# Optimization experiments

Hardware: AMD Instinct MI355X
Metric: run time of the kernel (lower is better)

The kernel has to match this reference:

```python
import jax, jax.numpy as jnp
import numpy as np

B = 512
D_MODEL = 512
D_STATE = 128
D_CONV = 2
EXPAND = 2
D_INNER = EXPAND * D_MODEL          # 1024
DT_RANK = (D_MODEL + 15) // 16      # 32 (mamba default 'auto')
HIDDEN = 256


def setup_inputs() -> dict:
    key = jax.random.key(0)
    ks = jax.random.split(key, 12)
    s = 0.02
    f32 = jnp.float32
    inp = {
        "x": jax.random.normal(ks[0], (B, D_MODEL), f32),
        # Mamba params (torch Linear weight layout: [out, in])
        "in_proj_w": jax.random.normal(ks[1], (2 * D_INNER, D_MODEL), f32) * s,
        "conv_w": jax.random.normal(ks[2], (D_INNER, D_CONV), f32) * s,  # depthwise kernel
        "conv_b": jnp.zeros((D_INNER,), f32),
        "x_proj_w": jax.random.normal(ks[3], (DT_RANK + 2 * D_STATE, D_INNER), f32) * s,
        "dt_proj_w": jax.random.normal(ks[4], (D_INNER, DT_RANK), f32) * s,
        "dt_proj_b": jax.random.normal(ks[5], (D_INNER,), f32) * s,
        "A_log": jnp.log(jnp.broadcast_to(
            jnp.arange(1, D_STATE + 1, dtype=f32), (D_INNER, D_STATE)).copy()),
        "D": jnp.ones((D_INNER,), f32),
        "out_proj_w": jax.random.normal(ks[6], (D_MODEL, D_INNER), f32) * s,
        # head params
        "fc1_w": jax.random.normal(ks[7], (HIDDEN, D_MODEL), f32) * s,
        "fc1_b": jnp.zeros((HIDDEN,), f32),
        "fc5_w": jax.random.normal(ks[8], (1, HIDDEN), f32) * s,
        "fc5_b": jnp.zeros((1,), f32),
    }
    return inp


def _mamba(x3, in_proj_w, conv_w, conv_b, x_proj_w, dt_proj_w, dt_proj_b,
           A_log, D, out_proj_w):
    # x3: [B, L, d_model]
    Bn, L, _ = x3.shape
    xz = jnp.einsum('bld,ed->ble', x3, in_proj_w)          # [B, L, 2*d_inner]
    xin, z = xz[..., :D_INNER], xz[..., D_INNER:]
    # depthwise causal conv1d (kernel D_CONV, padding D_CONV-1, truncated to L)
    xp = jnp.pad(xin, ((0, 0), (D_CONV - 1, 0), (0, 0)))
    conv = conv_b
    for k in range(D_CONV):
        conv = conv + conv_w[:, k] * xp[:, k:k + L, :]
    xin = jax.nn.silu(conv)                                 # [B, L, d_inner]
    x_dbl = jnp.einsum('blc,ec->ble', xin, x_proj_w)        # [B, L, dt_rank+2*d_state]
    dt = x_dbl[..., :DT_RANK]
    Bm = x_dbl[..., DT_RANK:DT_RANK + D_STATE]              # [B, L, d_state]
    Cm = x_dbl[..., DT_RANK + D_STATE:]                     # [B, L, d_state]
    dt = jax.nn.softplus(jnp.einsum('blr,cr->blc', dt, dt_proj_w) + dt_proj_b)
    A = -jnp.exp(A_log)                                     # [d_inner, d_state]
    dA = jnp.exp(dt[..., None] * A)                         # [B, L, d_inner, d_state]
    dBu = dt[..., None] * Bm[:, :, None, :] * xin[..., None]

    def step(h, t):
        dA_t, dBu_t, C_t = t
        h = dA_t * h + dBu_t                                # [B, d_inner, d_state]
        y_t = jnp.einsum('bcs,bs->bc', h, C_t)
        return h, y_t

    h0 = jnp.zeros((Bn, D_INNER, D_STATE), x3.dtype)
    _, ys = jax.lax.scan(step, h0, (dA.transpose(1, 0, 2, 3),
                                    dBu.transpose(1, 0, 2, 3),
                                    Cm.transpose(1, 0, 2)))
    y = ys.transpose(1, 0, 2)                               # [B, L, d_inner]
    y = (y + D * xin) * jax.nn.silu(z)
    return jnp.einsum('blc,dc->bld', y, out_proj_w)         # [B, L, d_model]


def reference(x, in_proj_w, conv_w, conv_b, x_proj_w, dt_proj_w, dt_proj_b,
              A_log, D, out_proj_w, fc1_w, fc1_b, fc5_w, fc5_b):
    h = _mamba(x[:, None, :], in_proj_w, conv_w, conv_b, x_proj_w,
               dt_proj_w, dt_proj_b, A_log, D, out_proj_w)[:, 0, :]
    h = h @ fc1_w.T + fc1_b
    h = jnp.where(h >= 0, h, 0.1 * h)   # LeakyReLU(0.1); dropout is eval-mode identity
    h = h @ fc5_w.T + fc5_b
    return jax.nn.sigmoid(h)            # [B, 1]
```

## Files before the change

kernel.cpp:

```cpp
#include <hip/hip_runtime.h>
#include <hip/hip_bf16.h>
#include <cstddef>

typedef __attribute__((ext_vector_type(8))) short short8;
typedef __attribute__((ext_vector_type(4))) float f32x4;

#define MFMA16(a, b, c) __builtin_amdgcn_mfma_f32_16x16x32_bf16((a), (b), (c), 0, 0, 0)

static __device__ __forceinline__ unsigned short f2bf(float f) {
    unsigned int u = __float_as_uint(f);
    u = (u + 0x7FFFu + ((u >> 16) & 1u)) >> 16;
    return (unsigned short)u;
}
static __device__ __forceinline__ float bf2f(unsigned short h) {
    return __uint_as_float(((unsigned int)h) << 16);
}
static __device__ __forceinline__ float silu_f(float v) { return v / (1.f + expf(-v)); }

enum : size_t {
    O_X    = 0,
    O_WIP  = O_X    + 512 * 512,
    O_WXP  = O_WIP  + 2048 * 512,
    O_WDT  = O_WXP  + 288 * 1024,
    O_WOUT = O_WDT  + 1024 * 32,
    O_WFC1 = O_WOUT + 512 * 1024,
    O_XIN  = O_WFC1 + 256 * 512,
    O_SZ   = O_XIN  + 512 * 1024,
    O_XDBL = O_SZ   + 512 * 1024,
    O_Y    = O_XDBL + 512 * 288,
    O_MOUT = O_Y    + 512 * 1024,
};

static __device__ __forceinline__ void cvt_seg(const float* __restrict__ s,
                                               unsigned short* __restrict__ d,
                                               int n, int gt, int np)
{
    for (int i = gt * 4; i < n; i += np * 4) {
        float4 v = *reinterpret_cast<const float4*>(s + i);
        ushort4 o;
        o.x = f2bf(v.x); o.y = f2bf(v.y); o.z = f2bf(v.z); o.w = f2bf(v.w);
        *reinterpret_cast<ushort4*>(d + i) = o;
    }
}

__global__ __launch_bounds__(256) void k_convert(
    const float* __restrict__ x,    const float* __restrict__ wip,
    const float* __restrict__ wxp,  const float* __restrict__ wdt,
    const float* __restrict__ wout, const float* __restrict__ wfc1,
    unsigned short* __restrict__ dst)
{
    const int gt = blockIdx.x * blockDim.x + threadIdx.x;
    const int np = gridDim.x * blockDim.x;
    cvt_seg(x,    dst + O_X,    512 * 512,  gt, np);
    cvt_seg(wip,  dst + O_WIP,  2048 * 512, gt, np);
    cvt_seg(wxp,  dst + O_WXP,  288 * 1024, gt, np);
    cvt_seg(wdt,  dst + O_WDT,  1024 * 32,  gt, np);
    cvt_seg(wout, dst + O_WOUT, 512 * 1024, gt, np);
    cvt_seg(wfc1, dst + O_WFC1, 256 * 512,  gt, np);
}

__global__ __launch_bounds__(256, 2) void k_s1(
    unsigned short* __restrict__ wsb,
    const float* __restrict__ cw, const float* __restrict__ cb)
{
    const int tid = threadIdx.x;
    const int w = tid >> 6, lane = tid & 63, l15 = lane & 15, g = lane >> 4;
    const int n0 = blockIdx.x * 64;
    const int m0 = blockIdx.y * 64 + w * 16;

    const unsigned short* ab = wsb + O_X   + (size_t)(m0 + l15) * 512 + g * 8;
    const unsigned short* bb = wsb + O_WIP + (size_t)(n0 + l15) * 512 + g * 8;

    f32x4 acc[4] = {};
#pragma unroll 4
    for (int k0 = 0; k0 < 512; k0 += 32) {
        short8 a = *reinterpret_cast<const short8*>(ab + k0);
#pragma unroll
        for (int f = 0; f < 4; ++f) {
            short8 b = *reinterpret_cast<const short8*>(bb + f * 16 * 512 + k0);
            acc[f] = MFMA16(a, b, acc[f]);
        }
    }

    const bool xhalf = (n0 < 1024);
    unsigned short* dst = wsb + (xhalf ? O_XIN : O_SZ);
#pragma unroll
    for (int f = 0; f < 4; ++f) {
        int n = n0 + f * 16 + l15;
        int c = xhalf ? n : n - 1024;
        float cwv = 0.f, cbv = 0.f;
        if (xhalf) { cwv = cw[2 * n + 1]; cbv = cb[n]; }
#pragma unroll
        for (int i = 0; i < 4; ++i) {
            int r = m0 + g * 4 + i;
            float v = acc[f][i];
            v = xhalf ? silu_f(cbv + cwv * v) : silu_f(v);
            dst[(size_t)r * 1024 + c] = f2bf(v);
        }
    }
}

__global__ __launch_bounds__(256, 2) void k_s2(unsigned short* __restrict__ wsb)
{
    const int tid = threadIdx.x;
    const int w = tid >> 6, lane = tid & 63, l15 = lane & 15, g = lane >> 4;
    const int n0 = blockIdx.x * 16;
    const int m0 = blockIdx.y * 64 + w * 16;

    const unsigned short* ab = wsb + O_XIN + (size_t)(m0 + l15) * 1024 + g * 8;
    const unsigned short* bb = wsb + O_WXP + (size_t)(n0 + l15) * 1024 + g * 8;

    f32x4 acc = {};
#pragma unroll 4
    for (int k0 = 0; k0 < 1024; k0 += 32) {
        short8 a = *reinterpret_cast<const short8*>(ab + k0);
        short8 b = *reinterpret_cast<const short8*>(bb + k0);
        acc = MFMA16(a, b, acc);
    }
    unsigned short* xd = wsb + O_XDBL;
#pragma unroll
    for (int i = 0; i < 4; ++i)
        xd[(size_t)(m0 + g * 4 + i) * 288 + n0 + l15] = f2bf(acc[i]);
}

__global__ __launch_bounds__(256, 2) void k_s3(
    unsigned short* __restrict__ wsb,
    const float* __restrict__ dtb, const float* __restrict__ Dv)
{
    __shared__ float bcp[16][17];
    __shared__ float bc_s[16];
    const int tid = threadIdx.x;
    const int w = tid >> 6, lane = tid & 63, l15 = lane & 15, g = lane >> 4;
    const int n0 = blockIdx.x * 256;
    const int m0 = blockIdx.y * 16;

    const unsigned short* xd = wsb + O_XDBL;
    {
        int r = tid >> 4, p = tid & 15;
        const unsigned short* row = xd + (size_t)(m0 + r) * 288;
        float s = 0.f;
#pragma unroll
        for (int q = 0; q < 8; ++q)
            s += bf2f(row[32 + p * 8 + q]) * bf2f(row[160 + p * 8 + q]);
        bcp[r][p] = s;
    }
    short8 a = *reinterpret_cast<const short8*>(xd + (size_t)(m0 + l15) * 288 + g * 8);
    __syncthreads();
    if (tid < 16) {
        float s = 0.f;
#pragma unroll
        for (int p = 0; p < 16; ++p) s += bcp[tid][p];
        bc_s[tid] = s;
    }
    __syncthreads();

    const unsigned short* wdtb = wsb + O_WDT;
    const unsigned short* xinb = wsb + O_XIN;
    const unsigned short* szb  = wsb + O_SZ;
    unsigned short* yb = wsb + O_Y;
    const f32x4 z4 = {0.f, 0.f, 0.f, 0.f};
#pragma unroll
    for (int f = 0; f < 4; ++f) {
        int n = n0 + w * 64 + f * 16 + l15;
        short8 b = *reinterpret_cast<const short8*>(wdtb + (size_t)n * 32 + g * 8);
        f32x4 acc = MFMA16(a, b, z4);
        float dtbv = dtb[n], Dvv = Dv[n];
#pragma unroll
        for (int i = 0; i < 4; ++i) {
            int r = m0 + g * 4 + i;
            float dtv = acc[i] + dtbv;
            dtv = (dtv > 20.f) ? dtv : log1pf(expf(dtv));
            float yv = bf2f(xinb[(size_t)r * 1024 + n]) *
                       (dtv * bc_s[g * 4 + i] + Dvv) *
                       bf2f(szb[(size_t)r * 1024 + n]);
            yb[(size_t)r * 1024 + n] = f2bf(yv);
        }
    }
}

__global__ __launch_bounds__(256, 2) void k_s4(unsigned short* __restrict__ wsb)
{
    const int tid = threadIdx.x;
    const int w = tid >> 6, lane = tid & 63, l15 = lane & 15, g = lane >> 4;
    const int n0 = blockIdx.x * 64 + w * 16;
    const int m0 = blockIdx.y * 16;

    const unsigned short* ab = wsb + O_Y    + (size_t)(m0 + l15) * 1024 + g * 8;
    const unsigned short* bb = wsb + O_WOUT + (size_t)(n0 + l15) * 1024 + g * 8;

    f32x4 acc = {};
#pragma unroll 4
    for (int k0 = 0; k0 < 1024; k0 += 32) {
        short8 a = *reinterpret_cast<const short8*>(ab + k0);
        short8 b = *reinterpret_cast<const short8*>(bb + k0);
        acc = MFMA16(a, b, acc);
    }
    unsigned short* mo = wsb + O_MOUT;
#pragma unroll
    for (int i = 0; i < 4; ++i)
        mo[(size_t)(m0 + g * 4 + i) * 512 + n0 + l15] = f2bf(acc[i]);
}

__global__ __launch_bounds__(256, 2) void k_s5(
    unsigned short* __restrict__ wsb,
    const float* __restrict__ bfc1, const float* __restrict__ wfc5,
    const float* __restrict__ bfc5, float* __restrict__ out)
{
    __shared__ float red[16][72];
    const int tid = threadIdx.x;
    const int w = tid >> 6, lane = tid & 63, l15 = lane & 15, g = lane >> 4;
    const int m0 = blockIdx.x * 16;

    const unsigned short* ab = wsb + O_MOUT + (size_t)(m0 + l15) * 512 + g * 8;
    const unsigned short* bb = wsb + O_WFC1 + (size_t)(w * 64 + l15) * 512 + g * 8;

    f32x4 acc[4] = {};
#pragma unroll 4
    for (int k0 = 0; k0 < 512; k0 += 32) {
        short8 a = *reinterpret_cast<const short8*>(ab + k0);
#pragma unroll
        for (int f = 0; f < 4; ++f) {
            short8 b = *reinterpret_cast<const short8*>(bb + f * 16 * 512 + k0);
            acc[f] = MFMA16(a, b, acc[f]);
        }
    }
    float part[4] = {0.f, 0.f, 0.f, 0.f};
#pragma unroll
    for (int f = 0; f < 4; ++f) {
        int n = w * 64 + f * 16 + l15;
        float b1 = bfc1[n], w5 = wfc5[n];
#pragma unroll
        for (int i = 0; i < 4; ++i) {
            float v = acc[f][i] + b1;
            v = v >= 0.f ? v : 0.1f * v;
            part[i] = fmaf(v, w5, part[i]);
        }
    }
#pragma unroll
    for (int i = 0; i < 4; ++i) red[g * 4 + i][w * 16 + l15] = part[i];
    __syncthreads();
    if (tid < 16) {
        float s = 0.f;
        for (int j = 0; j < 64; ++j) s += red[tid][j];
        out[m0 + tid] = 1.f / (1.f + expf(-(s + bfc5[0])));
    }
}

extern "C" void kernel_launch(void* const* d_in, const int* in_sizes, int n_in,
                              void* d_out, int out_size, void* d_ws, size_t ws_size,
                              hipStream_t stream)
{
    const float* x    = (const float*)d_in[0];
    const float* wip  = (const float*)d_in[1];
    const float* cw   = (const float*)d_in[2];
    const float* cb   = (const float*)d_in[3];
    const float* wxp  = (const float*)d_in[4];
    const float* wdt  = (const float*)d_in[5];
    const float* bdt  = (const float*)d_in[6];
    const float* Dv   = (const float*)d_in[8];
    const float* wout = (const float*)d_in[9];
    const float* wfc1 = (const float*)d_in[10];
    const float* bfc1 = (const float*)d_in[11];
    const float* wfc5 = (const float*)d_in[12];
    const float* bfc5 = (const float*)d_in[13];
    float* out = (float*)d_out;

    unsigned short* wsb = (unsigned short*)d_ws;

    k_convert<<<dim3(512),   256, 0, stream>>>(x, wip, wxp, wdt, wout, wfc1, wsb);
    k_s1     <<<dim3(32, 8), 256, 0, stream>>>(wsb, cw, cb);
    k_s2     <<<dim3(18, 8), 256, 0, stream>>>(wsb);
    k_s3     <<<dim3(4, 32), 256, 0, stream>>>(wsb, bdt, Dv);
    k_s4     <<<dim3(8, 32), 256, 0, stream>>>(wsb);
    k_s5     <<<dim3(32),    256, 0, stream>>>(wsb, bfc1, wfc5, bfc5, out);
}
```

Measured before the change: 147.7 us.

## Fuse fp32-to-bf16 conversion into GEMM loads and merge s3/s4 kernels

Removes the separate conversion kernel. Each GEMM now reads fp32 weights and inputs directly and packs them to bf16 in registers with v_cvt_pk_bf16_f32. The y computation (s3) is fused into the out_proj GEMM (s4) through an LDS tile, so y no longer round-trips through global memory and one launch is dropped. The head kernel moves to 512 threads with a shuffle reduction. The cost is that the fused kernel recomputes the dt/y tile in each of the 8 column blocks, and fp32 weights (twice the bytes) are re-read by many blocks instead of once.

```diff
diff --git a/kernel.cpp b/kernel.cpp
--- a/kernel.cpp
+++ b/kernel.cpp
@@ -17,67 +17,44 @@
 }
 static __device__ __forceinline__ float silu_f(float v) { return v / (1.f + expf(-v)); }
 
+static __device__ __forceinline__ short8 cvt_frag(const float* __restrict__ p) {
+    float4 a = *reinterpret_cast<const float4*>(p);
+    float4 b = *reinterpret_cast<const float4*>(p + 4);
+    union { short8 s; unsigned int u[4]; } r;
+    asm("v_cvt_pk_bf16_f32 %0, %1, %2" : "=v"(r.u[0]) : "v"(a.x), "v"(a.y));
+    asm("v_cvt_pk_bf16_f32 %0, %1, %2" : "=v"(r.u[1]) : "v"(a.z), "v"(a.w));
+    asm("v_cvt_pk_bf16_f32 %0, %1, %2" : "=v"(r.u[2]) : "v"(b.x), "v"(b.y));
+    asm("v_cvt_pk_bf16_f32 %0, %1, %2" : "=v"(r.u[3]) : "v"(b.z), "v"(b.w));
+    return r.s;
+}
+
 enum : size_t {
-    O_X    = 0,
-    O_WIP  = O_X    + 512 * 512,
-    O_WXP  = O_WIP  + 2048 * 512,
-    O_WDT  = O_WXP  + 288 * 1024,
-    O_WOUT = O_WDT  + 1024 * 32,
-    O_WFC1 = O_WOUT + 512 * 1024,
-    O_XIN  = O_WFC1 + 256 * 512,
+    O_XIN  = 0,
     O_SZ   = O_XIN  + 512 * 1024,
     O_XDBL = O_SZ   + 512 * 1024,
-    O_Y    = O_XDBL + 512 * 288,
-    O_MOUT = O_Y    + 512 * 1024,
+    O_MOUT = O_XDBL + 512 * 288,
 };
 
-static __device__ __forceinline__ void cvt_seg(const float* __restrict__ s,
-                                               unsigned short* __restrict__ d,
-                                               int n, int gt, int np)
-{
-    for (int i = gt * 4; i < n; i += np * 4) {
-        float4 v = *reinterpret_cast<const float4*>(s + i);
-        ushort4 o;
-        o.x = f2bf(v.x); o.y = f2bf(v.y); o.z = f2bf(v.z); o.w = f2bf(v.w);
-        *reinterpret_cast<ushort4*>(d + i) = o;
-    }
-}
-
-__global__ __launch_bounds__(256) void k_convert(
-    const float* __restrict__ x,    const float* __restrict__ wip,
-    const float* __restrict__ wxp,  const float* __restrict__ wdt,
-    const float* __restrict__ wout, const float* __restrict__ wfc1,
-    unsigned short* __restrict__ dst)
-{
-    const int gt = blockIdx.x * blockDim.x + threadIdx.x;
-    const int np = gridDim.x * blockDim.x;
-    cvt_seg(x,    dst + O_X,    512 * 512,  gt, np);
-    cvt_seg(wip,  dst + O_WIP,  2048 * 512, gt, np);
-    cvt_seg(wxp,  dst + O_WXP,  288 * 1024, gt, np);
-    cvt_seg(wdt,  dst + O_WDT,  1024 * 32,  gt, np);
-    cvt_seg(wout, dst + O_WOUT, 512 * 1024, gt, np);
-    cvt_seg(wfc1, dst + O_WFC1, 256 * 512,  gt, np);
-}
-
 __global__ __launch_bounds__(256, 2) void k_s1(
-    unsigned short* __restrict__ wsb,
-    const float* __restrict__ cw, const float* __restrict__ cb)
+    const float* __restrict__ x, const float* __restrict__ wip,
+    const float* __restrict__ cw, const float* __restrict__ cb,
+    unsigned short* __restrict__ wsb)
 {
     const int tid = threadIdx.x;
     const int w = tid >> 6, lane = tid & 63, l15 = lane & 15, g = lane >> 4;
     const int n0 = blockIdx.x * 64;
     const int m0 = blockIdx.y * 64 + w * 16;
 
-    const unsigned short* ab = wsb + O_X   + (size_t)(m0 + l15) * 512 + g * 8;
-    const unsigned short* bb = wsb + O_WIP + (size_t)(n0 + l15) * 512 + g * 8;
+    const float* arow = x   + (size_t)(m0 + l15) * 512 + g * 8;
+    const float* brow = wip + (size_t)(n0 + l15) * 512 + g * 8;
 
     f32x4 acc[4] = {};
 #pragma unroll 4
     for (int k0 = 0; k0 < 512; k0 += 32) {
-        short8 a = *reinterpret_cast<const short8*>(ab + k0);
+        short8 a = cvt_frag(arow + k0);
 #pragma unroll
         for (int f = 0; f < 4; ++f) {
-            short8 b = *reinterpret_cast<const short8*>(bb + f * 16 * 512 + k0);
+            short8 b = cvt_frag(brow + (size_t)f * 16 * 512 + k0);
             acc[f] = MFMA16(a, b, acc[f]);
         }
     }
@@ -100,7 +77,8 @@
     }
 }
 
-__global__ __launch_bounds__(256, 2) void k_s2(unsigned short* __restrict__ wsb)
+__global__ __launch_bounds__(256, 2) void k_s2(
+    const float* __restrict__ wxp, unsigned short* __restrict__ wsb)
 {
     const int tid = threadIdx.x;
     const int w = tid >> 6, lane = tid & 63, l15 = lane & 15, g = lane >> 4;
@@ -108,13 +86,13 @@
     const int m0 = blockIdx.y * 64 + w * 16;
 
     const unsigned short* ab = wsb + O_XIN + (size_t)(m0 + l15) * 1024 + g * 8;
-    const unsigned short* bb = wsb + O_WXP + (size_t)(n0 + l15) * 1024 + g * 8;
+    const float* brow = wxp + (size_t)(n0 + l15) * 1024 + g * 8;
 
     f32x4 acc = {};
 #pragma unroll 4
     for (int k0 = 0; k0 < 1024; k0 += 32) {
         short8 a = *reinterpret_cast<const short8*>(ab + k0);
-        short8 b = *reinterpret_cast<const short8*>(bb + k0);
+        short8 b = cvt_frag(brow + k0);
         acc = MFMA16(a, b, acc);
     }
     unsigned short* xd = wsb + O_XDBL;
@@ -123,15 +101,17 @@
         xd[(size_t)(m0 + g * 4 + i) * 288 + n0 + l15] = f2bf(acc[i]);
 }
 
-__global__ __launch_bounds__(256, 2) void k_s3(
-    unsigned short* __restrict__ wsb,
-    const float* __restrict__ dtb, const float* __restrict__ Dv)
-{
+__global__ __launch_bounds__(256, 2) void k_s34(
+    const float* __restrict__ wdt, const float* __restrict__ dtb,
+    const float* __restrict__ Dv,  const float* __restrict__ wout,
+    unsigned short* __restrict__ wsb)
+{
+    __shared__ __align__(16) unsigned short y_lds[16 * 1032];
     __shared__ float bcp[16][17];
     __shared__ float bc_s[16];
-    const int tid = threadIdx.x;
-    const int w = tid >> 6, lane = tid & 63, l15 = lane & 15, g = lane >> 4;
-    const int n0 = blockIdx.x * 256;
+
+    const int tid = threadIdx.x;
+    const int w = tid >> 6, lane = tid & 63, l15 = lane & 15, g = lane >> 4;
     const int m0 = blockIdx.y * 16;
 
     const unsigned short* xd = wsb + O_XDBL;
@@ -144,7 +124,7 @@
             s += bf2f(row[32 + p * 8 + q]) * bf2f(row[160 + p * 8 + q]);
         bcp[r][p] = s;
     }
-    short8 a = *reinterpret_cast<const short8*>(xd + (size_t)(m0 + l15) * 288 + g * 8);
+    short8 a3 = *reinterpret_cast<const short8*>(xd + (size_t)(m0 + l15) * 288 + g * 8);
     __syncthreads();
     if (tid < 16) {
         float s = 0.f;
@@ -154,45 +134,35 @@
     }
     __syncthreads();
 
-    const unsigned short* wdtb = wsb + O_WDT;
     const unsigned short* xinb = wsb + O_XIN;
     const unsigned short* szb  = wsb + O_SZ;
-    unsigned short* yb = wsb + O_Y;
     const f32x4 z4 = {0.f, 0.f, 0.f, 0.f};
 #pragma unroll
-    for (int f = 0; f < 4; ++f) {
-        int n = n0 + w * 64 + f * 16 + l15;
-        short8 b = *reinterpret_cast<const short8*>(wdtb + (size_t)n * 32 + g * 8);
-        f32x4 acc = MFMA16(a, b, z4);
+    for (int t = 0; t < 16; ++t) {
+        int n = (w * 16 + t) * 16 + l15;
+        short8 b = cvt_frag(wdt + (size_t)n * 32 + g * 8);
+        f32x4 acc = MFMA16(a3, b, z4);
         float dtbv = dtb[n], Dvv = Dv[n];
 #pragma unroll
         for (int i = 0; i < 4; ++i) {
-            int r = m0 + g * 4 + i;
+            int r = g * 4 + i;
             float dtv = acc[i] + dtbv;
             dtv = (dtv > 20.f) ? dtv : log1pf(expf(dtv));
-            float yv = bf2f(xinb[(size_t)r * 1024 + n]) *
-                       (dtv * bc_s[g * 4 + i] + Dvv) *
-                       bf2f(szb[(size_t)r * 1024 + n]);
-            yb[(size_t)r * 1024 + n] = f2bf(yv);
-        }
-    }
-}
-
-__global__ __launch_bounds__(256, 2) void k_s4(unsigned short* __restrict__ wsb)
-{
-    const int tid = threadIdx.x;
-    const int w = tid >> 6, lane = tid & 63, l15 = lane & 15, g = lane >> 4;
+            float yv = bf2f(xinb[(size_t)(m0 + r) * 1024 + n]) *
+                       (dtv * bc_s[r] + Dvv) *
+                       bf2f(szb[(size_t)(m0 + r) * 1024 + n]);
+            y_lds[r * 1032 + n] = f2bf(yv);
+        }
+    }
+    __syncthreads();
+
     const int n0 = blockIdx.x * 64 + w * 16;
-    const int m0 = blockIdx.y * 16;
-
-    const unsigned short* ab = wsb + O_Y    + (size_t)(m0 + l15) * 1024 + g * 8;
-    const unsigned short* bb = wsb + O_WOUT + (size_t)(n0 + l15) * 1024 + g * 8;
-
+    const float* brow = wout + (size_t)(n0 + l15) * 1024 + g * 8;
     f32x4 acc = {};
 #pragma unroll 4
     for (int k0 = 0; k0 < 1024; k0 += 32) {
-        short8 a = *reinterpret_cast<const short8*>(ab + k0);
-        short8 b = *reinterpret_cast<const short8*>(bb + k0);
+        short8 a = *reinterpret_cast<const short8*>(&y_lds[l15 * 1032 + k0 + g * 8]);
+        short8 b = cvt_frag(brow + k0);
         acc = MFMA16(a, b, acc);
     }
     unsigned short* mo = wsb + O_MOUT;
@@ -201,33 +171,33 @@
         mo[(size_t)(m0 + g * 4 + i) * 512 + n0 + l15] = f2bf(acc[i]);
 }
 
-__global__ __launch_bounds__(256, 2) void k_s5(
-    unsigned short* __restrict__ wsb,
-    const float* __restrict__ bfc1, const float* __restrict__ wfc5,
-    const float* __restrict__ bfc5, float* __restrict__ out)
-{
-    __shared__ float red[16][72];
+__global__ __launch_bounds__(512, 2) void k_s5(
+    const float* __restrict__ wfc1, const float* __restrict__ bfc1,
+    const float* __restrict__ wfc5, const float* __restrict__ bfc5,
+    unsigned short* __restrict__ wsb, float* __restrict__ out)
+{
+    __shared__ float red[16][8];
     const int tid = threadIdx.x;
     const int w = tid >> 6, lane = tid & 63, l15 = lane & 15, g = lane >> 4;
     const int m0 = blockIdx.x * 16;
 
     const unsigned short* ab = wsb + O_MOUT + (size_t)(m0 + l15) * 512 + g * 8;
-    const unsigned short* bb = wsb + O_WFC1 + (size_t)(w * 64 + l15) * 512 + g * 8;
-
-    f32x4 acc[4] = {};
+    const float* brow = wfc1 + (size_t)(w * 32 + l15) * 512 + g * 8;
+
+    f32x4 acc[2] = {};
 #pragma unroll 4
     for (int k0 = 0; k0 < 512; k0 += 32) {
         short8 a = *reinterpret_cast<const short8*>(ab + k0);
 #pragma unroll
-        for (int f = 0; f < 4; ++f) {
-            short8 b = *reinterpret_cast<const short8*>(bb + f * 16 * 512 + k0);
+        for (int f = 0; f < 2; ++f) {
+            short8 b = cvt_frag(brow + (size_t)f * 16 * 512 + k0);
             acc[f] = MFMA16(a, b, acc[f]);
         }
     }
     float part[4] = {0.f, 0.f, 0.f, 0.f};
 #pragma unroll
-    for (int f = 0; f < 4; ++f) {
-        int n = w * 64 + f * 16 + l15;
+    for (int f = 0; f < 2; ++f) {
+        int n = w * 32 + f * 16 + l15;
         float b1 = bfc1[n], w5 = wfc5[n];
 #pragma unroll
         for (int i = 0; i < 4; ++i) {
@@ -237,11 +207,17 @@
         }
     }
 #pragma unroll
-    for (int i = 0; i < 4; ++i) red[g * 4 + i][w * 16 + l15] = part[i];
+    for (int off = 1; off < 16; off <<= 1)
+#pragma unroll
+        for (int i = 0; i < 4; ++i) part[i] += __shfl_xor(part[i], off, 64);
+    if (l15 == 0)
+#pragma unroll
+        for (int i = 0; i < 4; ++i) red[g * 4 + i][w] = part[i];
     __syncthreads();
     if (tid < 16) {
         float s = 0.f;
-        for (int j = 0; j < 64; ++j) s += red[tid][j];
+#pragma unroll
+        for (int j = 0; j < 8; ++j) s += red[tid][j];
         out[m0 + tid] = 1.f / (1.f + expf(-(s + bfc5[0])));
     }
 }
@@ -267,10 +243,8 @@
 
     unsigned short* wsb = (unsigned short*)d_ws;
 
-    k_convert<<<dim3(512),   256, 0, stream>>>(x, wip, wxp, wdt, wout, wfc1, wsb);
-    k_s1     <<<dim3(32, 8), 256, 0, stream>>>(wsb, cw, cb);
-    k_s2     <<<dim3(18, 8), 256, 0, stream>>>(wsb);
-    k_s3     <<<dim3(4, 32), 256, 0, stream>>>(wsb, bdt, Dv);
-    k_s4     <<<dim3(8, 32), 256, 0, stream>>>(wsb);
-    k_s5     <<<dim3(32),    256, 0, stream>>>(wsb, bfc1, wfc5, bfc5, out);
-}
+    k_s1 <<<dim3(32, 8), 256, 0, stream>>>(x, wip, cw, cb, wsb);
+    k_s2 <<<dim3(18, 8), 256, 0, stream>>>(wxp, wsb);
+    k_s34<<<dim3(8, 32), 256, 0, stream>>>(wdt, bdt, Dv, wout, wsb);
+    k_s5 <<<dim3(32),    512, 0, stream>>>(wfc1, bfc1, wfc5, bfc5, wsb, out);
+}
```

Result: slower. 179.5 us (+21.5%).
